# Performance work log

Measured on AMD Instinct MI355X. Metric: run time of the kernel, lower is better.

Reference implementation:

```python
import jax, jax.numpy as jnp
import numpy as np
from math import ceil, log2

LEVELS = 6
N = 4096
DB4 = np.array([0.23037781330885523, 0.7148465705525415, 0.6308807679295904,
                -0.02798376941698385, -0.18703481171888114, 0.030841381835986965,
                0.032883011666982945, -0.010597401784997278], dtype=np.float32)


def setup_inputs() -> dict:
    key = jax.random.key(0)
    x = jax.random.normal(key, (N, N), dtype=jnp.float32)
    # learned filter bank: scaling.repeat(levels*2, 1)
    scaling = jnp.tile(jnp.asarray(DB4), (LEVELS * 2, 1))
    return {
        "x": x,
        "scaling": scaling,
        "alpha": jnp.float32(10.0),
        "b_plus": jnp.float32(2.0),
        "b_minus": jnp.float32(1.0),
    }


def compute_wavelet(h):
    # g_k = flip(h); odd indices negated
    g = jnp.flip(h, -1)
    sign = jnp.where(jnp.arange(g.shape[-1]) % 2 == 1, -1.0, 1.0).astype(g.dtype)
    return g * sign


def convolve(x, f, transpose=False):
    # circular convolution (or correlation if transpose) along last axis via FFT,
    # exactly as torch rfft/irfft with n=input_length
    L = x.shape[-1]
    fa = jnp.fft.rfft(x, axis=-1)
    fb = jnp.fft.rfft(f, n=L)
    if transpose:
        fb = jnp.conj(fb)
    return jnp.fft.irfft(fa * fb, n=L, axis=-1)


def forward_layer(x, h):
    w = compute_wavelet(h)
    return convolve(x, w)[:, ::2], convolve(x, h)[:, ::2]


def backward_layer(d, a, h):
    w = compute_wavelet(h)
    fd = jnp.zeros((d.shape[0], d.shape[1] * 2), d.dtype).at[:, ::2].set(d)
    fa = jnp.zeros((a.shape[0], a.shape[1] * 2), a.dtype).at[:, ::2].set(a)
    return convolve(fd, w, transpose=True) + convolve(fa, h, transpose=True)


def forward2d(x, hH, hV):
    d, a = forward_layer(x, hH)
    hh, hl = forward_layer(d.T, hV)
    hh, hl = hh.T, hl.T
    lh, ll = forward_layer(a.T, hV)
    lh, ll = lh.T, ll.T
    return (hh, hl, lh), ll


def backward2d(hh, hl, lh, ll, hH, hV):
    h = backward_layer(hh.T, hl.T, hV).T
    l = backward_layer(lh.T, ll.T, hV).T
    return backward_layer(h, l, hH)


def _despawn(x, scaling, alpha, b_plus, b_minus):
    n, m = x.shape
    pn = 2 ** ceil(log2(n)) - n
    pm = 2 ** ceil(log2(m)) - m
    xp = jnp.pad(x, ((0, pn), (0, pm)), mode="edge") if (pn or pm) else x

    approx = xp
    coeffs = []
    for lev in range(LEVELS):
        dets, approx = forward2d(approx, scaling[lev], scaling[lev + 1])
        coeffs.append(dets)

    def thr(t):
        return t * (jax.nn.sigmoid(alpha * (t - b_plus)) + jax.nn.sigmoid(-alpha * (t + b_minus)))

    filt = [tuple(thr(c) for c in tup) for tup in coeffs] + [thr(approx)]

    a = filt[-1]
    for lev in reversed(range(LEVELS)):
        hh, hl, lh = filt[lev]
        a = backward2d(hh, hl, lh, a, scaling[lev], scaling[lev + 1])

    flat = jnp.concatenate(
        [jnp.concatenate(tup, axis=-1).reshape(-1) for tup in filt[:-1]]
        + [filt[-1].reshape(-1)]
    )
    return a[:n, :m], flat


def reference(x, scaling, alpha, b_plus, b_minus):
    return _despawn(x, scaling, alpha, b_plus, b_minus)
```

## Files before the change

kernel.cpp:

```cpp
#include <hip/hip_runtime.h>
#include <hip/hip_bf16.h>


__device__ __forceinline__ float thrf(float t, float alpha, float bp, float bm) {
    float s1 = 1.0f / (1.0f + __expf(-alpha * (t - bp)));
    float s2 = 1.0f / (1.0f + __expf( alpha * (t + bm)));
    return t * (s1 + s2);
}

__device__ __forceinline__ void load_filt(const float* __restrict__ filt,
                                          float (&h)[8], float (&w)[8]) {
#pragma unroll
    for (int k = 0; k < 8; ++k) h[k] = filt[k];
#pragma unroll
    for (int k = 0; k < 8; ++k) w[k] = (k & 1) ? -h[7 - k] : h[7 - k];
}

__global__ __launch_bounds__(256) void fwd_fused(
    const float* __restrict__ X, int s, int sh,
    float* __restrict__ flat, float* __restrict__ All,
    const float* __restrict__ filt_row, const float* __restrict__ filt_col,
    const float* __restrict__ ap, const float* __restrict__ bpp,
    const float* __restrict__ bmp) {
    __shared__ float xs[72][73];
    __shared__ float Ds[72][33];
    __shared__ float As[72][33];
    const int tid = threadIdx.x;
    const int j0 = blockIdx.x * 32, i0 = blockIdx.y * 32;
    float hr[8], wr[8], hc[8], wc[8];
    load_filt(filt_row, hr, wr);
    load_filt(filt_col, hc, wc);
    const int sm = s - 1;
    for (int idx = tid; idx < 72 * 72; idx += 256) {
        int rr = idx / 72, cc = idx - rr * 72;
        int gr = (2 * i0 - 7 + rr) & sm;
        int gc = (2 * j0 - 7 + cc) & sm;
        xs[rr][cc] = X[(size_t)gr * s + gc];
    }
    __syncthreads();
    for (int idx = tid; idx < 72 * 32; idx += 256) {
        int rr = idx >> 5, j = idx & 31;
        float d = 0.f, a = 0.f;
#pragma unroll
        for (int k = 0; k < 8; ++k) {
            float v = xs[rr][2 * j + 7 - k];
            d += wr[k] * v;
            a += hr[k] * v;
        }
        Ds[rr][j] = d;
        As[rr][j] = a;
    }
    __syncthreads();
    const float alpha = *ap, bp = *bpp, bm = *bmp;
    for (int idx = tid; idx < 32 * 32; idx += 256) {
        int i = idx >> 5, j = idx & 31;
        float hh = 0.f, hl = 0.f, lh = 0.f, ll = 0.f;
#pragma unroll
        for (int k = 0; k < 8; ++k) {
            float dv = Ds[2 * i + 7 - k][j];
            float av = As[2 * i + 7 - k][j];
            hh += wc[k] * dv;
            hl += hc[k] * dv;
            lh += wc[k] * av;
            ll += hc[k] * av;
        }
        size_t ro = (size_t)(i0 + i) * (3 * sh) + (j0 + j);
        flat[ro]          = thrf(hh, alpha, bp, bm);
        flat[ro + sh]     = thrf(hl, alpha, bp, bm);
        flat[ro + 2 * sh] = thrf(lh, alpha, bp, bm);
        All[(size_t)(i0 + i) * sh + (j0 + j)] = ll;
    }
}

__global__ void thr_kernel(const float* __restrict__ in, float* __restrict__ out,
                           int n, const float* __restrict__ ap,
                           const float* __restrict__ bpp,
                           const float* __restrict__ bmp) {
    int idx = blockIdx.x * blockDim.x + threadIdx.x;
    if (idx >= n) return;
    out[idx] = thrf(in[idx], *ap, *bpp, *bmp);
}

__global__ __launch_bounds__(256) void inv_fused(
    const float* __restrict__ flatl, const float* __restrict__ a, int astride,
    int sc, float* __restrict__ outp, int ostride,
    const float* __restrict__ filt_col, const float* __restrict__ filt_row) {
    __shared__ float hhs[36][37], hls[36][37], lhs[36][37], as_[36][37];
    __shared__ float Hs[64][37], Ls[64][37];
    const int tid = threadIdx.x;
    const int m0 = blockIdx.x * 64, i0 = blockIdx.y * 64;
    float hr[8], wr[8], hc[8], wc[8];
    load_filt(filt_row, hr, wr);
    load_filt(filt_col, hc, wc);
    const int mm = sc - 1;
    const int r0 = i0 >> 1, c0 = m0 >> 1;
    const int ds = 3 * sc;
    for (int idx = tid; idx < 36 * 36; idx += 256) {
        int rr = idx / 36, cc = idx - rr * 36;
        int gr = (r0 + rr) & mm;
        int gc = (c0 + cc) & mm;
        size_t fo = (size_t)gr * ds + gc;
        hhs[rr][cc] = flatl[fo];
        hls[rr][cc] = flatl[fo + sc];
        lhs[rr][cc] = flatl[fo + 2 * sc];
        as_[rr][cc] = a[(size_t)gr * astride + gc];
    }
    __syncthreads();
    for (int idx = tid; idx < 64 * 36; idx += 256) {
        int n = idx / 36, jj = idx - (idx / 36) * 36;
        int nh = n >> 1;
        float Hv = 0.f, Lv = 0.f;
        if ((n & 1) == 0) {
#pragma unroll
            for (int t = 0; t < 4; ++t) {
                int lr = nh + t;
                Hv += wc[2 * t] * hhs[lr][jj] + hc[2 * t] * hls[lr][jj];
                Lv += wc[2 * t] * lhs[lr][jj] + hc[2 * t] * as_[lr][jj];
            }
        } else {
#pragma unroll
            for (int t = 0; t < 4; ++t) {
                int lr = nh + t + 1;
                Hv += wc[2 * t + 1] * hhs[lr][jj] + hc[2 * t + 1] * hls[lr][jj];
                Lv += wc[2 * t + 1] * lhs[lr][jj] + hc[2 * t + 1] * as_[lr][jj];
            }
        }
        Hs[n][jj] = Hv;
        Ls[n][jj] = Lv;
    }
    __syncthreads();
    for (int idx = tid; idx < 64 * 64; idx += 256) {
        int i = idx >> 6, m = idx & 63;
        int mh = m >> 1;
        float acc = 0.f;
        if ((m & 1) == 0) {
#pragma unroll
            for (int t = 0; t < 4; ++t) {
                int lc = mh + t;
                acc += wr[2 * t] * Hs[i][lc] + hr[2 * t] * Ls[i][lc];
            }
        } else {
#pragma unroll
            for (int t = 0; t < 4; ++t) {
                int lc = mh + t + 1;
                acc += wr[2 * t + 1] * Hs[i][lc] + hr[2 * t + 1] * Ls[i][lc];
            }
        }
        outp[(size_t)(i0 + i) * ostride + (m0 + m)] = acc;
    }
}

extern "C" void kernel_launch(void* const* d_in, const int* in_sizes, int n_in,
                              void* d_out, int out_size, void* d_ws, size_t ws_size,
                              hipStream_t stream) {
    const float* x    = (const float*)d_in[0];
    const float* scal = (const float*)d_in[1];
    const float* ap   = (const float*)d_in[2];
    const float* bp   = (const float*)d_in[3];
    const float* bm   = (const float*)d_in[4];
    float* out = (float*)d_out;
    float* ws  = (float*)d_ws;

    const int N = 4096;
    float* recon = out;
    float* flat  = out + 16777216;

    static const size_t Aoff[7] = {0, 0, 4194304, 5242880, 5505024, 5570560, 5586944};
    static const size_t flatOff[6] = {0, 12582912, 15728640, 16515072, 16711680, 16760832};
    const size_t finalOff = 16773120;
    float* P0 = ws + 5591040;
    float* P1 = ws + 5591040 + 4194304;

    dim3 blk(256);

    const float* src = x;
    for (int lev = 0; lev < 6; ++lev) {
        int s = N >> lev, sh = s >> 1;
        dim3 g(sh / 32, sh / 32);
        fwd_fused<<<g, blk, 0, stream>>>(src, s, sh, flat + flatOff[lev],
                                         ws + Aoff[lev + 1],
                                         scal + lev * 8, scal + (lev + 1) * 8,
                                         ap, bp, bm);
        src = ws + Aoff[lev + 1];
    }
    thr_kernel<<<dim3(16), blk, 0, stream>>>(ws + Aoff[6], flat + finalOff, 4096,
                                             ap, bp, bm);

    const float* a_in = flat + finalOff;
    for (int lev = 5; lev >= 0; --lev) {
        int sc = N >> (lev + 1), r = 2 * sc;
        float* outp = (lev == 0) ? recon : ((lev & 1) ? P1 : P0);
        dim3 g(r / 64, r / 64);
        inv_fused<<<g, blk, 0, stream>>>(flat + flatOff[lev], a_in, sc,
                                         sc, outp, r,
                                         scal + (lev + 1) * 8, scal + lev * 8);
        a_in = outp;
    }
}
```

Measured before the change: 342.1 us.

## Collapse small wavelet levels into one persistent kernel with grid barriers

Replaces the thirteen per-level launches with three: a full-grid kernel for the first forward level, one persistent 256-block kernel that runs forward levels 1-5 and inverse levels 5-1 tile-strided with atomic grid barriers between levels, and a full-grid kernel for the last inverse level. The final threshold on the coarsest approximation is folded into the level-5 forward pass, so the separate threshold kernel goes away. The aim is to remove launch overhead and tail idle time on the small levels. In exchange it relies on all 256 blocks being co-resident for the spin barrier, adds a memset per call, and runs the small levels with fewer blocks.

```diff
diff --git a/kernel.cpp b/kernel.cpp
--- a/kernel.cpp
+++ b/kernel.cpp
@@ -1,6 +1,8 @@
 #include <hip/hip_runtime.h>
 #include <hip/hip_bf16.h>
 
+
+#define NBLK_SMALL 256
 
 __device__ __forceinline__ float thrf(float t, float alpha, float bp, float bm) {
     float s1 = 1.0f / (1.0f + __expf(-alpha * (t - bp)));
@@ -16,138 +18,210 @@
     for (int k = 0; k < 8; ++k) w[k] = (k & 1) ? -h[7 - k] : h[7 - k];
 }
 
-__global__ __launch_bounds__(256) void fwd_fused(
-    const float* __restrict__ X, int s, int sh,
-    float* __restrict__ flat, float* __restrict__ All,
-    const float* __restrict__ filt_row, const float* __restrict__ filt_col,
-    const float* __restrict__ ap, const float* __restrict__ bpp,
-    const float* __restrict__ bmp) {
-    __shared__ float xs[72][73];
-    __shared__ float Ds[72][33];
-    __shared__ float As[72][33];
+__device__ void fwd_tiles(const float* __restrict__ X, int s, int sh,
+                          float* __restrict__ flat, float* __restrict__ All,
+                          float* __restrict__ thrA,
+                          const float* __restrict__ frow,
+                          const float* __restrict__ fcol,
+                          float alpha, float bp, float bm,
+                          float* smem, int tstart, int tstep) {
+    float hr[8], wr[8], hc[8], wc[8];
+    load_filt(frow, hr, wr);
+    load_filt(fcol, hc, wc);
+    float* xs = smem;
+    float* Ds = smem + 5256;
+    float* As = smem + 7632;
     const int tid = threadIdx.x;
-    const int j0 = blockIdx.x * 32, i0 = blockIdx.y * 32;
+    const int sm = s - 1;
+    const int ntx = sh >> 5;
+    const int ntiles = ntx * ntx;
+    const int shft = __builtin_ctz(ntx);
+    for (int t = tstart; t < ntiles; t += tstep) {
+        const int i0 = (t >> shft) * 32, j0 = (t & (ntx - 1)) * 32;
+        for (int idx = tid; idx < 72 * 72; idx += 256) {
+            int rr = idx / 72, cc = idx - rr * 72;
+            xs[rr * 73 + cc] =
+                X[(size_t)((2 * i0 - 7 + rr) & sm) * s + ((2 * j0 - 7 + cc) & sm)];
+        }
+        __syncthreads();
+        for (int idx = tid; idx < 72 * 32; idx += 256) {
+            int rr = idx >> 5, j = idx & 31;
+            float d = 0.f, a = 0.f;
+#pragma unroll
+            for (int k = 0; k < 8; ++k) {
+                float v = xs[rr * 73 + 2 * j + 7 - k];
+                d += wr[k] * v;
+                a += hr[k] * v;
+            }
+            Ds[rr * 33 + j] = d;
+            As[rr * 33 + j] = a;
+        }
+        __syncthreads();
+        for (int idx = tid; idx < 32 * 32; idx += 256) {
+            int i = idx >> 5, j = idx & 31;
+            float hh = 0.f, hl = 0.f, lh = 0.f, ll = 0.f;
+#pragma unroll
+            for (int k = 0; k < 8; ++k) {
+                float dv = Ds[(2 * i + 7 - k) * 33 + j];
+                float av = As[(2 * i + 7 - k) * 33 + j];
+                hh += wc[k] * dv;
+                hl += hc[k] * dv;
+                lh += wc[k] * av;
+                ll += hc[k] * av;
+            }
+            size_t ro = (size_t)(i0 + i) * (3 * sh) + (j0 + j);
+            flat[ro]          = thrf(hh, alpha, bp, bm);
+            flat[ro + sh]     = thrf(hl, alpha, bp, bm);
+            flat[ro + 2 * sh] = thrf(lh, alpha, bp, bm);
+            size_t ao = (size_t)(i0 + i) * sh + (j0 + j);
+            if (All)  All[ao]  = ll;
+            if (thrA) thrA[ao] = thrf(ll, alpha, bp, bm);
+        }
+        __syncthreads();
+    }
+}
+
+__device__ void inv_tiles(const float* __restrict__ flatl,
+                          const float* __restrict__ a, int sc,
+                          float* __restrict__ outp, int ostride,
+                          const float* __restrict__ fcol,
+                          const float* __restrict__ frow,
+                          float* smem, int tstart, int tstep) {
     float hr[8], wr[8], hc[8], wc[8];
-    load_filt(filt_row, hr, wr);
-    load_filt(filt_col, hc, wc);
-    const int sm = s - 1;
-    for (int idx = tid; idx < 72 * 72; idx += 256) {
-        int rr = idx / 72, cc = idx - rr * 72;
-        int gr = (2 * i0 - 7 + rr) & sm;
-        int gc = (2 * j0 - 7 + cc) & sm;
-        xs[rr][cc] = X[(size_t)gr * s + gc];
-    }
+    load_filt(frow, hr, wr);
+    load_filt(fcol, hc, wc);
+    float* hhs = smem;
+    float* hls = smem + 1332;
+    float* lhs = smem + 2664;
+    float* as_ = smem + 3996;
+    float* Hs  = smem + 5328;
+    float* Ls  = smem + 7696;
+    const int tid = threadIdx.x;
+    const int mm = sc - 1;
+    const int r = 2 * sc;
+    const int ntx = r >> 6;
+    const int ntiles = ntx * ntx;
+    const int shft = __builtin_ctz(ntx);
+    const int ds = 3 * sc;
+    for (int t = tstart; t < ntiles; t += tstep) {
+        const int i0 = (t >> shft) * 64, m0 = (t & (ntx - 1)) * 64;
+        const int r0 = i0 >> 1, c0 = m0 >> 1;
+        for (int idx = tid; idx < 36 * 36; idx += 256) {
+            int rr = idx / 36, cc = idx - rr * 36;
+            int gr = (r0 + rr) & mm, gc = (c0 + cc) & mm;
+            size_t fo = (size_t)gr * ds + gc;
+            hhs[rr * 37 + cc] = flatl[fo];
+            hls[rr * 37 + cc] = flatl[fo + sc];
+            lhs[rr * 37 + cc] = flatl[fo + 2 * sc];
+            as_[rr * 37 + cc] = a[(size_t)gr * sc + gc];
+        }
+        __syncthreads();
+        for (int idx = tid; idx < 64 * 36; idx += 256) {
+            int n = idx / 36, jj = idx - n * 36;
+            int nh = n >> 1;
+            float Hv = 0.f, Lv = 0.f;
+            if ((n & 1) == 0) {
+#pragma unroll
+                for (int tt = 0; tt < 4; ++tt) {
+                    int lr = (nh + tt) * 37 + jj;
+                    Hv += wc[2 * tt] * hhs[lr] + hc[2 * tt] * hls[lr];
+                    Lv += wc[2 * tt] * lhs[lr] + hc[2 * tt] * as_[lr];
+                }
+            } else {
+#pragma unroll
+                for (int tt = 0; tt < 4; ++tt) {
+                    int lr = (nh + tt + 1) * 37 + jj;
+                    Hv += wc[2 * tt + 1] * hhs[lr] + hc[2 * tt + 1] * hls[lr];
+                    Lv += wc[2 * tt + 1] * lhs[lr] + hc[2 * tt + 1] * as_[lr];
+                }
+            }
+            Hs[n * 37 + jj] = Hv;
+            Ls[n * 37 + jj] = Lv;
+        }
+        __syncthreads();
+        for (int idx = tid; idx < 64 * 64; idx += 256) {
+            int i = idx >> 6, m = idx & 63;
+            int mh = m >> 1;
+            float acc = 0.f;
+            if ((m & 1) == 0) {
+#pragma unroll
+                for (int tt = 0; tt < 4; ++tt) {
+                    int lc = mh + tt;
+                    acc += wr[2 * tt] * Hs[i * 37 + lc] + hr[2 * tt] * Ls[i * 37 + lc];
+                }
+            } else {
+#pragma unroll
+                for (int tt = 0; tt < 4; ++tt) {
+                    int lc = mh + tt + 1;
+                    acc += wr[2 * tt + 1] * Hs[i * 37 + lc] + hr[2 * tt + 1] * Ls[i * 37 + lc];
+                }
+            }
+            outp[(size_t)(i0 + i) * ostride + (m0 + m)] = acc;
+        }
+        __syncthreads();
+    }
+}
+
+__device__ __forceinline__ void grid_barrier(unsigned* c, unsigned target) {
     __syncthreads();
-    for (int idx = tid; idx < 72 * 32; idx += 256) {
-        int rr = idx >> 5, j = idx & 31;
-        float d = 0.f, a = 0.f;
-#pragma unroll
-        for (int k = 0; k < 8; ++k) {
-            float v = xs[rr][2 * j + 7 - k];
-            d += wr[k] * v;
-            a += hr[k] * v;
-        }
-        Ds[rr][j] = d;
-        As[rr][j] = a;
+    if (threadIdx.x == 0) {
+        __hip_atomic_fetch_add(c, 1u, __ATOMIC_RELEASE, __HIP_MEMORY_SCOPE_AGENT);
+        while (__hip_atomic_load(c, __ATOMIC_ACQUIRE, __HIP_MEMORY_SCOPE_AGENT) < target) {
+            __builtin_amdgcn_s_sleep(1);
+        }
     }
     __syncthreads();
+}
+
+__global__ __launch_bounds__(256) void fwd0_kernel(
+    const float* __restrict__ X, float* __restrict__ flat, float* __restrict__ A1,
+    const float* __restrict__ scal, const float* __restrict__ ap,
+    const float* __restrict__ bpp, const float* __restrict__ bmp) {
+    __shared__ float smem[10064];
+    fwd_tiles(X, 4096, 2048, flat, A1, nullptr, scal, scal + 8,
+              *ap, *bpp, *bmp, smem, blockIdx.x, gridDim.x);
+}
+
+__global__ __launch_bounds__(256) void small_levels_kernel(
+    float* __restrict__ ws, float* __restrict__ out,
+    const float* __restrict__ scal, const float* __restrict__ ap,
+    const float* __restrict__ bpp, const float* __restrict__ bmp,
+    unsigned* __restrict__ counter) {
+    __shared__ float smem[10064];
     const float alpha = *ap, bp = *bpp, bm = *bmp;
-    for (int idx = tid; idx < 32 * 32; idx += 256) {
-        int i = idx >> 5, j = idx & 31;
-        float hh = 0.f, hl = 0.f, lh = 0.f, ll = 0.f;
-#pragma unroll
-        for (int k = 0; k < 8; ++k) {
-            float dv = Ds[2 * i + 7 - k][j];
-            float av = As[2 * i + 7 - k][j];
-            hh += wc[k] * dv;
-            hl += hc[k] * dv;
-            lh += wc[k] * av;
-            ll += hc[k] * av;
-        }
-        size_t ro = (size_t)(i0 + i) * (3 * sh) + (j0 + j);
-        flat[ro]          = thrf(hh, alpha, bp, bm);
-        flat[ro + sh]     = thrf(hl, alpha, bp, bm);
-        flat[ro + 2 * sh] = thrf(lh, alpha, bp, bm);
-        All[(size_t)(i0 + i) * sh + (j0 + j)] = ll;
-    }
-}
-
-__global__ void thr_kernel(const float* __restrict__ in, float* __restrict__ out,
-                           int n, const float* __restrict__ ap,
-                           const float* __restrict__ bpp,
-                           const float* __restrict__ bmp) {
-    int idx = blockIdx.x * blockDim.x + threadIdx.x;
-    if (idx >= n) return;
-    out[idx] = thrf(in[idx], *ap, *bpp, *bmp);
-}
-
-__global__ __launch_bounds__(256) void inv_fused(
-    const float* __restrict__ flatl, const float* __restrict__ a, int astride,
-    int sc, float* __restrict__ outp, int ostride,
-    const float* __restrict__ filt_col, const float* __restrict__ filt_row) {
-    __shared__ float hhs[36][37], hls[36][37], lhs[36][37], as_[36][37];
-    __shared__ float Hs[64][37], Ls[64][37];
-    const int tid = threadIdx.x;
-    const int m0 = blockIdx.x * 64, i0 = blockIdx.y * 64;
-    float hr[8], wr[8], hc[8], wc[8];
-    load_filt(filt_row, hr, wr);
-    load_filt(filt_col, hc, wc);
-    const int mm = sc - 1;
-    const int r0 = i0 >> 1, c0 = m0 >> 1;
-    const int ds = 3 * sc;
-    for (int idx = tid; idx < 36 * 36; idx += 256) {
-        int rr = idx / 36, cc = idx - rr * 36;
-        int gr = (r0 + rr) & mm;
-        int gc = (c0 + cc) & mm;
-        size_t fo = (size_t)gr * ds + gc;
-        hhs[rr][cc] = flatl[fo];
-        hls[rr][cc] = flatl[fo + sc];
-        lhs[rr][cc] = flatl[fo + 2 * sc];
-        as_[rr][cc] = a[(size_t)gr * astride + gc];
-    }
-    __syncthreads();
-    for (int idx = tid; idx < 64 * 36; idx += 256) {
-        int n = idx / 36, jj = idx - (idx / 36) * 36;
-        int nh = n >> 1;
-        float Hv = 0.f, Lv = 0.f;
-        if ((n & 1) == 0) {
-#pragma unroll
-            for (int t = 0; t < 4; ++t) {
-                int lr = nh + t;
-                Hv += wc[2 * t] * hhs[lr][jj] + hc[2 * t] * hls[lr][jj];
-                Lv += wc[2 * t] * lhs[lr][jj] + hc[2 * t] * as_[lr][jj];
-            }
-        } else {
-#pragma unroll
-            for (int t = 0; t < 4; ++t) {
-                int lr = nh + t + 1;
-                Hv += wc[2 * t + 1] * hhs[lr][jj] + hc[2 * t + 1] * hls[lr][jj];
-                Lv += wc[2 * t + 1] * lhs[lr][jj] + hc[2 * t + 1] * as_[lr][jj];
-            }
-        }
-        Hs[n][jj] = Hv;
-        Ls[n][jj] = Lv;
-    }
-    __syncthreads();
-    for (int idx = tid; idx < 64 * 64; idx += 256) {
-        int i = idx >> 6, m = idx & 63;
-        int mh = m >> 1;
-        float acc = 0.f;
-        if ((m & 1) == 0) {
-#pragma unroll
-            for (int t = 0; t < 4; ++t) {
-                int lc = mh + t;
-                acc += wr[2 * t] * Hs[i][lc] + hr[2 * t] * Ls[i][lc];
-            }
-        } else {
-#pragma unroll
-            for (int t = 0; t < 4; ++t) {
-                int lc = mh + t + 1;
-                acc += wr[2 * t + 1] * Hs[i][lc] + hr[2 * t + 1] * Ls[i][lc];
-            }
-        }
-        outp[(size_t)(i0 + i) * ostride + (m0 + m)] = acc;
-    }
+    float* flat = out + 16777216;
+    const size_t Aoff[6]    = {0, 0, 4194304, 5242880, 5505024, 5570560};
+    const size_t Ioff[6]    = {0, 6979584, 5931008, 5668864, 5603328, 5586944};
+    const size_t flatOff[6] = {0, 12582912, 15728640, 16515072, 16711680, 16760832};
+    const size_t finalOff = 16773120;
+    unsigned phase = 0;
+    for (int lev = 1; lev <= 5; ++lev) {
+        int s = 4096 >> lev, sh = s >> 1;
+        fwd_tiles(ws + Aoff[lev], s, sh, flat + flatOff[lev],
+                  (lev < 5) ? (ws + Aoff[lev + 1]) : nullptr,
+                  (lev == 5) ? (flat + finalOff) : nullptr,
+                  scal + lev * 8, scal + (lev + 1) * 8,
+                  alpha, bp, bm, smem, blockIdx.x, gridDim.x);
+        grid_barrier(counter, (++phase) * NBLK_SMALL);
+    }
+    const float* a_in = flat + finalOff;
+    for (int lev = 5; lev >= 1; --lev) {
+        int sc = 4096 >> (lev + 1);
+        float* outp = ws + Ioff[lev];
+        inv_tiles(flat + flatOff[lev], a_in, sc, outp, 2 * sc,
+                  scal + (lev + 1) * 8, scal + lev * 8,
+                  smem, blockIdx.x, gridDim.x);
+        if (lev > 1) grid_barrier(counter, (++phase) * NBLK_SMALL);
+        a_in = outp;
+    }
+}
+
+__global__ __launch_bounds__(256) void inv0_kernel(
+    const float* __restrict__ flatl, const float* __restrict__ a,
+    float* __restrict__ recon, const float* __restrict__ scal) {
+    __shared__ float smem[10064];
+    inv_tiles(flatl, a, 2048, recon, 4096, scal + 8, scal,
+              smem, blockIdx.x, gridDim.x);
 }
 
 extern "C" void kernel_launch(void* const* d_in, const int* in_sizes, int n_in,
@@ -161,39 +235,17 @@
     float* out = (float*)d_out;
     float* ws  = (float*)d_ws;
 
-    const int N = 4096;
-    float* recon = out;
-    float* flat  = out + 16777216;
-
-    static const size_t Aoff[7] = {0, 0, 4194304, 5242880, 5505024, 5570560, 5586944};
-    static const size_t flatOff[6] = {0, 12582912, 15728640, 16515072, 16711680, 16760832};
-    const size_t finalOff = 16773120;
-    float* P0 = ws + 5591040;
-    float* P1 = ws + 5591040 + 4194304;
-
-    dim3 blk(256);
-
-    const float* src = x;
-    for (int lev = 0; lev < 6; ++lev) {
-        int s = N >> lev, sh = s >> 1;
-        dim3 g(sh / 32, sh / 32);
-        fwd_fused<<<g, blk, 0, stream>>>(src, s, sh, flat + flatOff[lev],
-                                         ws + Aoff[lev + 1],
-                                         scal + lev * 8, scal + (lev + 1) * 8,
-                                         ap, bp, bm);
-        src = ws + Aoff[lev + 1];
-    }
-    thr_kernel<<<dim3(16), blk, 0, stream>>>(ws + Aoff[6], flat + finalOff, 4096,
-                                             ap, bp, bm);
-
-    const float* a_in = flat + finalOff;
-    for (int lev = 5; lev >= 0; --lev) {
-        int sc = N >> (lev + 1), r = 2 * sc;
-        float* outp = (lev == 0) ? recon : ((lev & 1) ? P1 : P0);
-        dim3 g(r / 64, r / 64);
-        inv_fused<<<g, blk, 0, stream>>>(flat + flatOff[lev], a_in, sc,
-                                         sc, outp, r,
-                                         scal + (lev + 1) * 8, scal + lev * 8);
-        a_in = outp;
-    }
-}
+    float* flat = out + 16777216;
+    unsigned* counter = (unsigned*)(ws + 11173888);
+
+    hipMemsetAsync(counter, 0, sizeof(unsigned), stream);
+
+    fwd0_kernel<<<dim3(64 * 64), dim3(256), 0, stream>>>(
+        x, flat, ws , scal, ap, bp, bm);
+
+    small_levels_kernel<<<dim3(NBLK_SMALL), dim3(256), 0, stream>>>(
+        ws, out, scal, ap, bp, bm, counter);
+
+    inv0_kernel<<<dim3(32 * 32), dim3(256), 0, stream>>>(
+        flat, ws + 6979584, out, scal);
+}
```

Result: slower. 500.2 us (+46.2%).
